# Kernel tuning notes

Hardware: AMD Instinct MI355X
Metric: run time of the kernel (lower is better)

Reference implementation:

```python
import jax, jax.numpy as jnp
import numpy as np

E, T, H, I = 16, 512, 1024, 4096


def setup_inputs() -> dict:
    key = jax.random.key(0)
    k_x, k_w1, k_b1, k_w2, k_b2 = jax.random.split(key, 5)
    scale = 0.02
    return {
        "route_results": jax.random.normal(k_x, (E, T, H), dtype=jnp.float32),
        "W1": jax.random.normal(k_w1, (E, H, I), dtype=jnp.float32) * scale,
        "b1": jax.random.normal(k_b1, (E, I), dtype=jnp.float32) * scale,
        "W2": jax.random.normal(k_w2, (E, I, H), dtype=jnp.float32) * scale,
        "b2": jax.random.normal(k_b2, (E, H), dtype=jnp.float32) * scale,
    }


def reference(route_results, W1, b1, W2, b2):
    # Per-expert 2-layer linear MLP (no activation in source), expressed as
    # a single grouped (batched) GEMM over the expert axis e.
    h = jnp.einsum("eth,ehi->eti", route_results, W1) + b1[:, None, :]
    y = jnp.einsum("eti,eih->eth", h, W2) + b2[:, None, :]
    # torch.cat(expert_results, dim=0): stack expert outputs along token dim.
    e, t, hid = y.shape
    return y.reshape(e * t, hid)
```

## Files before the change

### kernel.cpp

```cpp
#include <hip/hip_runtime.h>
#include <stdint.h>


#define E_ 16
#define T_ 512
#define H_ 1024
#define I_ 4096

typedef _Float16 f16x8 __attribute__((ext_vector_type(8)));
typedef __fp16   h2    __attribute__((ext_vector_type(2)));
typedef float    f32x4 __attribute__((ext_vector_type(4)));

#define LDK 40

template <bool A_IS_F16, bool OUT_IS_F16>
__global__ __launch_bounds__(256, 2) void moe_gemm(const void* __restrict__ Aall,
                                                   const float* __restrict__ Ball,
                                                   const float* __restrict__ biasAll,
                                                   void* __restrict__ Call,
                                                   int M, int N, int K) {
    __shared__ _Float16 sA[128 * LDK];
    __shared__ _Float16 sB[128 * LDK];

    const int e   = blockIdx.z;
    const int m0  = blockIdx.y * 128;
    const int n0  = blockIdx.x * 128;
    const int tid = threadIdx.x;
    const int lane = tid & 63;
    const int wave = tid >> 6;
    const int wm = (wave >> 1) * 64;
    const int wn = (wave & 1) * 64;
    const int lrow = lane & 15;
    const int lk8  = (lane >> 4) * 8;

    const float* B_e    = Ball + (size_t)e * K * N;
    const float* bias_e = biasAll + (size_t)e * N;
    const float*     A_f32 = (const float*)Aall + (size_t)e * M * K;
    const _Float16*  A_f16 = (const _Float16*)Aall + (size_t)e * M * K;

    const int bn  = ((tid >> 6) & 1) * 64 + (tid & 63);
    const int bkh = (tid >> 7) * 16;
    const int ar = (tid >> 6) * 32 + ((tid & 63) >> 2);
    const int ak = (tid & 3) * 8;
    const int r  = tid >> 2;
    const int c8 = (tid & 3) * 8;

    float bv[16];
    f32x4 a32[4];
    f16x8 a16[2];

    auto load_tile = [&](int k0) {
        const float* bsrc = B_e + (size_t)(k0 + bkh) * N + n0 + bn;
#pragma unroll
        for (int kk = 0; kk < 16; ++kk)
            bv[kk] = bsrc[(size_t)kk * N];
        if (A_IS_F16) {
            a16[0] = *(const f16x8*)(A_f16 + (size_t)(m0 + r) * K + k0 + c8);
            a16[1] = *(const f16x8*)(A_f16 + (size_t)(m0 + r + 64) * K + k0 + c8);
        } else {
            const float* a0 = A_f32 + (size_t)(m0 + ar) * K + k0 + ak;
            a32[0] = *(const f32x4*)a0;
            a32[1] = *(const f32x4*)(a0 + 4);
            const float* a1 = A_f32 + (size_t)(m0 + ar + 16) * K + k0 + ak;
            a32[2] = *(const f32x4*)a1;
            a32[3] = *(const f32x4*)(a1 + 4);
        }
    };

    auto store_tile = [&]() {
        f16x8 w0, w1;
#pragma unroll
        for (int j = 0; j < 4; ++j) {
            ((h2*)&w0)[j] = __builtin_amdgcn_cvt_pkrtz(bv[2 * j],     bv[2 * j + 1]);
            ((h2*)&w1)[j] = __builtin_amdgcn_cvt_pkrtz(bv[8 + 2 * j], bv[8 + 2 * j + 1]);
        }
        *(f16x8*)&sB[bn * LDK + bkh]     = w0;
        *(f16x8*)&sB[bn * LDK + bkh + 8] = w1;
        if (A_IS_F16) {
            *(f16x8*)&sA[r * LDK + c8]        = a16[0];
            *(f16x8*)&sA[(r + 64) * LDK + c8] = a16[1];
        } else {
#pragma unroll
            for (int p = 0; p < 2; ++p) {
                f16x8 w;
                ((h2*)&w)[0] = __builtin_amdgcn_cvt_pkrtz(a32[2 * p].x, a32[2 * p].y);
                ((h2*)&w)[1] = __builtin_amdgcn_cvt_pkrtz(a32[2 * p].z, a32[2 * p].w);
                ((h2*)&w)[2] = __builtin_amdgcn_cvt_pkrtz(a32[2 * p + 1].x, a32[2 * p + 1].y);
                ((h2*)&w)[3] = __builtin_amdgcn_cvt_pkrtz(a32[2 * p + 1].z, a32[2 * p + 1].w);
                *(f16x8*)&sA[(ar + p * 16) * LDK + ak] = w;
            }
        }
    };

    f32x4 acc[4][4];
    const f32x4 zero = {0.f, 0.f, 0.f, 0.f};
#pragma unroll
    for (int i = 0; i < 4; ++i)
#pragma unroll
        for (int j = 0; j < 4; ++j) acc[i][j] = zero;

    load_tile(0);

    for (int k0 = 0; k0 < K; k0 += 32) {
        __syncthreads();
        store_tile();
        if (k0 + 32 < K)
            load_tile(k0 + 32);
        __syncthreads();

        f16x8 af[4], bf[4];
#pragma unroll
        for (int mi = 0; mi < 4; ++mi)
            af[mi] = *(const f16x8*)&sA[(wm + mi * 16 + lrow) * LDK + lk8];
#pragma unroll
        for (int ni = 0; ni < 4; ++ni)
            bf[ni] = *(const f16x8*)&sB[(wn + ni * 16 + lrow) * LDK + lk8];
#pragma unroll
        for (int mi = 0; mi < 4; ++mi)
#pragma unroll
            for (int ni = 0; ni < 4; ++ni)
                acc[mi][ni] = __builtin_amdgcn_mfma_f32_16x16x32_f16(af[mi], bf[ni], acc[mi][ni], 0, 0, 0);
    }

    const int row_base = (lane >> 4) * 4;
#pragma unroll
    for (int ni = 0; ni < 4; ++ni) {
        const int n = n0 + wn + ni * 16 + lrow;
        const float bv2 = bias_e[n];
#pragma unroll
        for (int mi = 0; mi < 4; ++mi) {
            const int mbase = m0 + wm + mi * 16 + row_base;
#pragma unroll
            for (int rr = 0; rr < 4; ++rr) {
                const float val = acc[mi][ni][rr] + bv2;
                const size_t idx = (size_t)e * M * N + (size_t)(mbase + rr) * N + n;
                if (OUT_IS_F16)
                    ((_Float16*)Call)[idx] = (_Float16)val;
                else
                    ((float*)Call)[idx] = val;
            }
        }
    }
}

extern "C" void kernel_launch(void* const* d_in, const int* in_sizes, int n_in,
                              void* d_out, int out_size, void* d_ws, size_t ws_size,
                              hipStream_t stream) {
    (void)in_sizes; (void)n_in; (void)out_size; (void)ws_size;
    const float* x  = (const float*)d_in[0];
    const float* W1 = (const float*)d_in[1];
    const float* b1 = (const float*)d_in[2];
    const float* W2 = (const float*)d_in[3];
    const float* b2 = (const float*)d_in[4];
    float* out = (float*)d_out;
    _Float16* hbuf = (_Float16*)d_ws;

    dim3 blk(256, 1, 1);
    dim3 g1(I_ / 128, T_ / 128, E_);
    moe_gemm<false, true><<<g1, blk, 0, stream>>>((const void*)x, W1, b1, (void*)hbuf, T_, I_, H_);
    dim3 g2(H_ / 128, T_ / 128, E_);
    moe_gemm<true, false><<<g2, blk, 0, stream>>>((const void*)hbuf, W2, b2, (void*)out, T_, H_, I_);
}
```

Measured before the change: 705.9 us.

## Double-buffer LDS tiles and overlap tile stores with MFMA compute

Shared-memory A/B tiles become two buffers, so the next tile is converted and stored into the alternate buffer while the current one is consumed. The store and the next global prefetch are placed between two halves of the MFMA loop, and the loop needs only one barrier per iteration instead of two. The aim is to hide LDS store and conversion latency behind compute and to cut synchronisation. It doubles LDS use to about 40 KB per block, which may reduce occupancy.

```diff
diff --git a/kernel.cpp b/kernel.cpp
--- a/kernel.cpp
+++ b/kernel.cpp
@@ -19,8 +19,8 @@
                                                    const float* __restrict__ biasAll,
                                                    void* __restrict__ Call,
                                                    int M, int N, int K) {
-    __shared__ _Float16 sA[128 * LDK];
-    __shared__ _Float16 sB[128 * LDK];
+    __shared__ _Float16 sA[2][128 * LDK];
+    __shared__ _Float16 sB[2][128 * LDK];
 
     const int e   = blockIdx.z;
     const int m0  = blockIdx.y * 128;
@@ -67,18 +67,18 @@
         }
     };
 
-    auto store_tile = [&]() {
+    auto store_tile = [&](_Float16* dA, _Float16* dB) {
         f16x8 w0, w1;
 #pragma unroll
         for (int j = 0; j < 4; ++j) {
             ((h2*)&w0)[j] = __builtin_amdgcn_cvt_pkrtz(bv[2 * j],     bv[2 * j + 1]);
             ((h2*)&w1)[j] = __builtin_amdgcn_cvt_pkrtz(bv[8 + 2 * j], bv[8 + 2 * j + 1]);
         }
-        *(f16x8*)&sB[bn * LDK + bkh]     = w0;
-        *(f16x8*)&sB[bn * LDK + bkh + 8] = w1;
+        *(f16x8*)&dB[bn * LDK + bkh]     = w0;
+        *(f16x8*)&dB[bn * LDK + bkh + 8] = w1;
         if (A_IS_F16) {
-            *(f16x8*)&sA[r * LDK + c8]        = a16[0];
-            *(f16x8*)&sA[(r + 64) * LDK + c8] = a16[1];
+            *(f16x8*)&dA[r * LDK + c8]        = a16[0];
+            *(f16x8*)&dA[(r + 64) * LDK + c8] = a16[1];
         } else {
 #pragma unroll
             for (int p = 0; p < 2; ++p) {
@@ -87,7 +87,7 @@
                 ((h2*)&w)[1] = __builtin_amdgcn_cvt_pkrtz(a32[2 * p].z, a32[2 * p].w);
                 ((h2*)&w)[2] = __builtin_amdgcn_cvt_pkrtz(a32[2 * p + 1].x, a32[2 * p + 1].y);
                 ((h2*)&w)[3] = __builtin_amdgcn_cvt_pkrtz(a32[2 * p + 1].z, a32[2 * p + 1].w);
-                *(f16x8*)&sA[(ar + p * 16) * LDK + ak] = w;
+                *(f16x8*)&dA[(ar + p * 16) * LDK + ak] = w;
             }
         }
     };
@@ -99,27 +99,45 @@
 #pragma unroll
         for (int j = 0; j < 4; ++j) acc[i][j] = zero;
 
+    const int nt = K / 32;
+
     load_tile(0);
+    store_tile(sA[0], sB[0]);
+    load_tile(32);
+    __syncthreads();
 
-    for (int k0 = 0; k0 < K; k0 += 32) {
-        __syncthreads();
-        store_tile();
-        if (k0 + 32 < K)
-            load_tile(k0 + 32);
-        __syncthreads();
+    for (int t = 0; t < nt; ++t) {
+        const int cur = t & 1;
+        const _Float16* rA = sA[cur];
+        const _Float16* rB = sB[cur];
 
         f16x8 af[4], bf[4];
 #pragma unroll
         for (int mi = 0; mi < 4; ++mi)
-            af[mi] = *(const f16x8*)&sA[(wm + mi * 16 + lrow) * LDK + lk8];
+            af[mi] = *(const f16x8*)&rA[(wm + mi * 16 + lrow) * LDK + lk8];
 #pragma unroll
         for (int ni = 0; ni < 4; ++ni)
-            bf[ni] = *(const f16x8*)&sB[(wn + ni * 16 + lrow) * LDK + lk8];
+            bf[ni] = *(const f16x8*)&rB[(wn + ni * 16 + lrow) * LDK + lk8];
+
 #pragma unroll
-        for (int mi = 0; mi < 4; ++mi)
+        for (int mi = 0; mi < 2; ++mi)
 #pragma unroll
             for (int ni = 0; ni < 4; ++ni)
                 acc[mi][ni] = __builtin_amdgcn_mfma_f32_16x16x32_f16(af[mi], bf[ni], acc[mi][ni], 0, 0, 0);
+
+        if (t + 1 < nt) {
+            store_tile(sA[cur ^ 1], sB[cur ^ 1]);
+            if (t + 2 < nt)
+                load_tile((t + 2) * 32);
+        }
+
+#pragma unroll
+        for (int mi = 2; mi < 4; ++mi)
+#pragma unroll
+            for (int ni = 0; ni < 4; ++ni)
+                acc[mi][ni] = __builtin_amdgcn_mfma_f32_16x16x32_f16(af[mi], bf[ni], acc[mi][ni], 0, 0, 0);
+
+        __syncthreads();
     }
 
     const int row_base = (lane >> 4) * 4;
```

Result: no change. 697.4 us (-1.2%).
